# Kernel optimization log

Hardware: AMD Instinct MI355X
Metric: run time of the kernel (lower is better)

Reference implementation:

```python
import jax, jax.numpy as jnp
import numpy as np

EPSILON = 0.1
MAX_ITERATIONS = 100


def setup_inputs() -> dict:
    key = jax.random.key(0)
    k1, k2 = jax.random.split(key)
    x = jax.random.normal(k1, (16, 3, 2048), dtype=jnp.float32)
    y = jax.random.normal(k2, (16, 3, 2048), dtype=jnp.float32)
    return {"x": x, "y": y}


def reference(x, y):
    # x, y: (B, D, N) channels-first point clouds -> (B, N, D)
    xt = jnp.swapaxes(x, 1, 2)
    yt = jnp.swapaxes(y, 1, 2)
    B, N, _ = xt.shape
    # squared euclidean cost: (B, N, N)
    x2 = jnp.sum(xt * xt, axis=-1)  # (B, N)
    y2 = jnp.sum(yt * yt, axis=-1)  # (B, N)
    C = x2[:, :, None] + y2[:, None, :] - 2.0 * jnp.einsum('bnd,bmd->bnm', xt, yt)
    C = jnp.maximum(C, 0.0)  # cdist clamps negatives from cancellation
    K = jnp.exp(-C / EPSILON)

    inv_n = 1.0 / N
    u0 = jnp.full((B, N), inv_n, dtype=x.dtype)
    v0 = jnp.full((B, N), inv_n, dtype=x.dtype)

    def step(carry, _):
        u, _v = carry
        v = inv_n / (jnp.einsum('bnm,bn->bm', K, u) + 1e-8)  # K^T u
        u = inv_n / (jnp.einsum('bnm,bm->bn', K, v) + 1e-8)  # K v
        return (u, v), None

    (u, v), _ = jax.lax.scan(step, (u0, v0), None, length=MAX_ITERATIONS)
    # sum(plan * C) / B where plan = u[:,:,None] * K * v[:,None,:]
    return jnp.einsum('bn,bnm,bm->', u, K * C, v) / B
```

## Files before the change

kernel.cpp:

```cpp
#include <hip/hip_runtime.h>

#define NB 16
#define NN 2048
#define G  64
#define ITERS 100

typedef float v2f __attribute__((ext_vector_type(2)));

static constexpr float INV_N = 1.0f / (float)NN;
static constexpr float NEG_INV_EPS = -10.0f;

__device__ __forceinline__ float fastrcp(float x) { return __builtin_amdgcn_rcpf(x); }

__device__ __forceinline__ void dec4(unsigned int u, float& f0, float& f1, float& f2, float& f3) {
    v2f lo = __builtin_amdgcn_cvt_pk_f32_fp8((int)u, false);
    v2f hi = __builtin_amdgcn_cvt_pk_f32_fp8((int)u, true);
    f0 = lo[0]; f1 = lo[1]; f2 = hi[0]; f3 = hi[1];
}

__global__ __launch_bounds__(256) void build_K(const float* __restrict__ x,
                                               const float* __restrict__ y,
                                               unsigned char* __restrict__ K8,
                                               float* __restrict__ INVS) {
    const int n = blockIdx.x, b = blockIdx.y, tid = threadIdx.x;
    const int w = tid >> 6, l = tid & 63;
    const float* xb = x + (size_t)b * 3 * NN;
    const float* yb = y + (size_t)b * 3 * NN;
    const float x0 = xb[n], x1 = xb[NN + n], x2 = xb[2 * NN + n];
    const float xs = x0 * x0 + x1 * x1 + x2 * x2;
    const int m0 = tid * 8;

    const float4 a0 = *(const float4*)(yb + m0);
    const float4 a1 = *(const float4*)(yb + m0 + 4);
    const float4 b0 = *(const float4*)(yb + NN + m0);
    const float4 b1 = *(const float4*)(yb + NN + m0 + 4);
    const float4 c0 = *(const float4*)(yb + 2 * NN + m0);
    const float4 c1 = *(const float4*)(yb + 2 * NN + m0 + 4);
    const float yy0[8] = {a0.x, a0.y, a0.z, a0.w, a1.x, a1.y, a1.z, a1.w};
    const float yy1[8] = {b0.x, b0.y, b0.z, b0.w, b1.x, b1.y, b1.z, b1.w};
    const float yy2[8] = {c0.x, c0.y, c0.z, c0.w, c1.x, c1.y, c1.z, c1.w};

    float k[8];
#pragma unroll
    for (int j = 0; j < 8; ++j) {
        const float ys  = yy0[j] * yy0[j] + yy1[j] * yy1[j] + yy2[j] * yy2[j];
        const float dot = x0 * yy0[j] + x1 * yy1[j] + x2 * yy2[j];
        const float C   = fmaxf(xs + ys - 2.0f * dot, 0.0f);
        k[j] = __expf(NEG_INV_EPS * C);
    }

    float mx = fmaxf(fmaxf(fmaxf(k[0], k[1]), fmaxf(k[2], k[3])),
                     fmaxf(fmaxf(k[4], k[5]), fmaxf(k[6], k[7])));
#pragma unroll
    for (int off = 32; off > 0; off >>= 1) mx = fmaxf(mx, __shfl_xor(mx, off, 64));
    __shared__ float red[4];
    if (l == 0) red[w] = mx;
    __syncthreads();
    mx = fmaxf(fmaxf(red[0], red[1]), fmaxf(red[2], red[3]));
    mx = fmaxf(mx, 1e-30f);
    const int e = (int)((__float_as_uint(mx) >> 23) & 0xffu) - 127;
    const float sc = __uint_as_float((unsigned)(127 - e) << 23);
    if (tid == 0) INVS[b * NN + n] = __uint_as_float((unsigned)(127 + e) << 23);

    int p0 = __builtin_amdgcn_cvt_pk_fp8_f32(k[0] * sc, k[1] * sc, 0, false);
    p0     = __builtin_amdgcn_cvt_pk_fp8_f32(k[2] * sc, k[3] * sc, p0, true);
    int p1 = __builtin_amdgcn_cvt_pk_fp8_f32(k[4] * sc, k[5] * sc, 0, false);
    p1     = __builtin_amdgcn_cvt_pk_fp8_f32(k[6] * sc, k[7] * sc, p1, true);
    uint2 pk; pk.x = (unsigned)p0; pk.y = (unsigned)p1;
    *(uint2*)(K8 + ((size_t)(b * NN + n)) * NN + m0) = pk;
}

__global__ __launch_bounds__(256) void reduce_v(const float* __restrict__ PART,
                                                float* __restrict__ VV) {
    const int t = blockIdx.x * 256 + threadIdx.x;
    const int b = t >> 9;
    const int m4 = (t & 511) << 2;
    const float* p = PART + (size_t)(b * G) * NN + m4;
    float s0 = 0, s1 = 0, s2 = 0, s3 = 0;
#pragma unroll 8
    for (int g = 0; g < G; ++g) {
        const float4 q = *(const float4*)(p + (size_t)g * NN);
        s0 += q.x; s1 += q.y; s2 += q.z; s3 += q.w;
    }
    float4 o;
    o.x = INV_N * fastrcp(s0 + 1e-8f);
    o.y = INV_N * fastrcp(s1 + 1e-8f);
    o.z = INV_N * fastrcp(s2 + 1e-8f);
    o.w = INV_N * fastrcp(s3 + 1e-8f);
    *(float4*)(VV + (size_t)b * NN + m4) = o;
}

#define DOT16(kk, vv) {                                                        \
    float f0_, f1_, f2_, f3_;                                                  \
    dec4(kk.x, f0_, f1_, f2_, f3_);                                            \
    d0 = fmaf(f0_, vv[0], d0);  d1 = fmaf(f1_, vv[1], d1);                     \
    d2 = fmaf(f2_, vv[2], d2);  d3 = fmaf(f3_, vv[3], d3);                     \
    dec4(kk.y, f0_, f1_, f2_, f3_);                                            \
    d0 = fmaf(f0_, vv[4], d0);  d1 = fmaf(f1_, vv[5], d1);                     \
    d2 = fmaf(f2_, vv[6], d2);  d3 = fmaf(f3_, vv[7], d3);                     \
    dec4(kk.z, f0_, f1_, f2_, f3_);                                            \
    d0 = fmaf(f0_, vv[8], d0);  d1 = fmaf(f1_, vv[9], d1);                     \
    d2 = fmaf(f2_, vv[10], d2); d3 = fmaf(f3_, vv[11], d3);                    \
    dec4(kk.w, f0_, f1_, f2_, f3_);                                            \
    d0 = fmaf(f0_, vv[12], d0); d1 = fmaf(f1_, vv[13], d1);                    \
    d2 = fmaf(f2_, vv[14], d2); d3 = fmaf(f3_, vv[15], d3); }

#define ACC16(kk, aa, uu) {                                                    \
    float f0_, f1_, f2_, f3_;                                                  \
    dec4(kk.x, f0_, f1_, f2_, f3_);                                            \
    aa[0] = fmaf(f0_, uu, aa[0]);   aa[1] = fmaf(f1_, uu, aa[1]);              \
    aa[2] = fmaf(f2_, uu, aa[2]);   aa[3] = fmaf(f3_, uu, aa[3]);              \
    dec4(kk.y, f0_, f1_, f2_, f3_);                                            \
    aa[4] = fmaf(f0_, uu, aa[4]);   aa[5] = fmaf(f1_, uu, aa[5]);              \
    aa[6] = fmaf(f2_, uu, aa[6]);   aa[7] = fmaf(f3_, uu, aa[7]);              \
    dec4(kk.z, f0_, f1_, f2_, f3_);                                            \
    aa[8] = fmaf(f0_, uu, aa[8]);   aa[9] = fmaf(f1_, uu, aa[9]);              \
    aa[10] = fmaf(f2_, uu, aa[10]); aa[11] = fmaf(f3_, uu, aa[11]);            \
    dec4(kk.w, f0_, f1_, f2_, f3_);                                            \
    aa[12] = fmaf(f0_, uu, aa[12]); aa[13] = fmaf(f1_, uu, aa[13]);            \
    aa[14] = fmaf(f2_, uu, aa[14]); aa[15] = fmaf(f3_, uu, aa[15]); }

__global__ __launch_bounds__(256) void fused_pass(const unsigned char* __restrict__ K8,
                                                  const float* __restrict__ VV,
                                                  const float* __restrict__ INVS,
                                                  float* __restrict__ u_out,
                                                  float* __restrict__ PART,
                                                  int first) {
    const int g = blockIdx.x, b = blockIdx.y, tid = threadIdx.x;
    const int w = tid >> 6, l = tid & 63;

    float v[2][16];
    if (!first) {
        const float* vb = VV + b * NN + l * 16;
#pragma unroll
        for (int h = 0; h < 2; ++h) {
            const float4 q0 = *(const float4*)(vb + h * 1024);
            const float4 q1 = *(const float4*)(vb + h * 1024 + 4);
            const float4 q2 = *(const float4*)(vb + h * 1024 + 8);
            const float4 q3 = *(const float4*)(vb + h * 1024 + 12);
            v[h][0]  = q0.x; v[h][1]  = q0.y; v[h][2]  = q0.z; v[h][3]  = q0.w;
            v[h][4]  = q1.x; v[h][5]  = q1.y; v[h][6]  = q1.z; v[h][7]  = q1.w;
            v[h][8]  = q2.x; v[h][9]  = q2.y; v[h][10] = q2.z; v[h][11] = q2.w;
            v[h][12] = q3.x; v[h][13] = q3.y; v[h][14] = q3.z; v[h][15] = q3.w;
        }
    }

    float acc0[16], acc1[16];
#pragma unroll
    for (int j = 0; j < 16; ++j) { acc0[j] = 0.0f; acc1[j] = 0.0f; }

    const int row0 = g * 32 + w * 8;
    const unsigned char* Kb = K8 + ((size_t)(b * NN + row0)) * NN + l * 16;
    const float* invp = INVS + b * NN + row0;

#pragma unroll
    for (int rp = 0; rp < 4; ++rp) {
        const unsigned char* pA = Kb + (size_t)(2 * rp) * NN;
        const unsigned char* pB = pA + NN;
        const uint4 kA0 = *(const uint4*)(pA);
        const uint4 kA1 = *(const uint4*)(pA + 1024);
        const uint4 kB0 = *(const uint4*)(pB);
        const uint4 kB1 = *(const uint4*)(pB + 1024);
        const float invsA = invp[2 * rp];
        const float invsB = invp[2 * rp + 1];

        float uwA, uwB;
        if (first) {
            uwA = INV_N * invsA;
            uwB = INV_N * invsB;
        } else {
            float d0 = 0, d1 = 0, d2 = 0, d3 = 0;
            DOT16(kA0, v[0]); DOT16(kA1, v[1]);
            float dA = (d0 + d1) + (d2 + d3);
            d0 = 0; d1 = 0; d2 = 0; d3 = 0;
            DOT16(kB0, v[0]); DOT16(kB1, v[1]);
            float dB = (d0 + d1) + (d2 + d3);
#pragma unroll
            for (int off = 32; off > 0; off >>= 1) {
                dA += __shfl_xor(dA, off, 64);
                dB += __shfl_xor(dB, off, 64);
            }
            uwA = INV_N * fastrcp(dA * invsA + 1e-8f) * invsA;
            uwB = INV_N * fastrcp(dB * invsB + 1e-8f) * invsB;
        }
        if (l == 0) {
            u_out[b * NN + row0 + 2 * rp]     = uwA;
            u_out[b * NN + row0 + 2 * rp + 1] = uwB;
        }
        ACC16(kA0, acc0, uwA); ACC16(kA1, acc1, uwA);
        ACC16(kB0, acc0, uwB); ACC16(kB1, acc1, uwB);
    }

    __shared__ float lds[4][NN];
    {
        float* dst = &lds[w][l * 16];
        *(float4*)(dst)          = make_float4(acc0[0],  acc0[1],  acc0[2],  acc0[3]);
        *(float4*)(dst + 4)      = make_float4(acc0[4],  acc0[5],  acc0[6],  acc0[7]);
        *(float4*)(dst + 8)      = make_float4(acc0[8],  acc0[9],  acc0[10], acc0[11]);
        *(float4*)(dst + 12)     = make_float4(acc0[12], acc0[13], acc0[14], acc0[15]);
        *(float4*)(dst + 1024)      = make_float4(acc1[0],  acc1[1],  acc1[2],  acc1[3]);
        *(float4*)(dst + 1024 + 4)  = make_float4(acc1[4],  acc1[5],  acc1[6],  acc1[7]);
        *(float4*)(dst + 1024 + 8)  = make_float4(acc1[8],  acc1[9],  acc1[10], acc1[11]);
        *(float4*)(dst + 1024 + 12) = make_float4(acc1[12], acc1[13], acc1[14], acc1[15]);
    }
    __syncthreads();
    float o[8];
#pragma unroll
    for (int j = 0; j < 8; ++j)
        o[j] = (lds[0][tid * 8 + j] + lds[1][tid * 8 + j]) +
               (lds[2][tid * 8 + j] + lds[3][tid * 8 + j]);
    float* p = PART + ((size_t)(b * G + g)) * NN + tid * 8;
    *(float4*)(p)     = make_float4(o[0], o[1], o[2], o[3]);
    *(float4*)(p + 4) = make_float4(o[4], o[5], o[6], o[7]);
}

__global__ __launch_bounds__(256) void final_sum(const unsigned char* __restrict__ K8,
                                                 const float* __restrict__ x,
                                                 const float* __restrict__ y,
                                                 const float* __restrict__ VV,
                                                 const float* __restrict__ u_in,
                                                 float* __restrict__ out) {
    const int g = blockIdx.x, b = blockIdx.y, tid = threadIdx.x;
    const int w = tid >> 6, l = tid & 63;
    const float* vb = VV + b * NN;

    float v[4][8];
#pragma unroll
    for (int s = 0; s < 4; ++s) {
        const float4 p0 = *(const float4*)(vb + s * 512 + l * 8);
        const float4 p1 = *(const float4*)(vb + s * 512 + l * 8 + 4);
        v[s][0] = p0.x; v[s][1] = p0.y; v[s][2] = p0.z; v[s][3] = p0.w;
        v[s][4] = p1.x; v[s][5] = p1.y; v[s][6] = p1.z; v[s][7] = p1.w;
    }

    const float* xb = x + (size_t)b * 3 * NN;
    const float* yb = y + (size_t)b * 3 * NN;
    float lacc = 0.0f;

    for (int r = 0; r < 8; ++r) {
        const int n = g * 32 + w * 8 + r;
        const float x0 = xb[n], x1 = xb[NN + n], x2 = xb[2 * NN + n];
        const float xs = x0 * x0 + x1 * x1 + x2 * x2;
        const float uwn = u_in[b * NN + n];
        const unsigned char* Kp = K8 + ((size_t)(b * NN + n)) * NN + l * 8;
        float racc = 0.0f;
#pragma unroll
        for (int s = 0; s < 4; ++s) {
            const int m0 = s * 512 + l * 8;
            const uint2 kv = *(const uint2*)(Kp + s * 512);
            float ky[8];
            dec4(kv.x, ky[0], ky[1], ky[2], ky[3]);
            dec4(kv.y, ky[4], ky[5], ky[6], ky[7]);
            const float4 a0 = *(const float4*)(yb + m0);
            const float4 a1 = *(const float4*)(yb + m0 + 4);
            const float4 b0 = *(const float4*)(yb + NN + m0);
            const float4 b1 = *(const float4*)(yb + NN + m0 + 4);
            const float4 c0 = *(const float4*)(yb + 2 * NN + m0);
            const float4 c1 = *(const float4*)(yb + 2 * NN + m0 + 4);
            const float yy0[8] = {a0.x, a0.y, a0.z, a0.w, a1.x, a1.y, a1.z, a1.w};
            const float yy1[8] = {b0.x, b0.y, b0.z, b0.w, b1.x, b1.y, b1.z, b1.w};
            const float yy2[8] = {c0.x, c0.y, c0.z, c0.w, c1.x, c1.y, c1.z, c1.w};
#pragma unroll
            for (int j = 0; j < 8; ++j) {
                const float ys  = yy0[j] * yy0[j] + yy1[j] * yy1[j] + yy2[j] * yy2[j];
                const float dot = x0 * yy0[j] + x1 * yy1[j] + x2 * yy2[j];
                const float C   = fmaxf(xs + ys - 2.0f * dot, 0.0f);
                racc = fmaf(ky[j] * C, v[s][j], racc);
            }
        }
        lacc = fmaf(uwn, racc, lacc);
    }
#pragma unroll
    for (int off = 32; off > 0; off >>= 1) lacc += __shfl_xor(lacc, off, 64);
    __shared__ float red[4];
    if (l == 0) red[w] = lacc;
    __syncthreads();
    if (tid == 0) atomicAdd(out, (red[0] + red[1] + red[2] + red[3]) * (1.0f / (float)NB));
}

extern "C" void kernel_launch(void* const* d_in, const int* in_sizes, int n_in,
                              void* d_out, int out_size, void* d_ws, size_t ws_size,
                              hipStream_t stream) {
    const float* x = (const float*)d_in[0];
    const float* y = (const float*)d_in[1];
    float* out = (float*)d_out;
    char* ws = (char*)d_ws;

    unsigned char* K8 = (unsigned char*)ws;
    const size_t KBYTES = (size_t)NB * NN * NN;
    float* PART = (float*)(ws + KBYTES);
    const size_t PARTN = (size_t)NB * G * NN;
    float* VV   = PART + PARTN;
    float* ub   = VV + (size_t)NB * NN;
    float* INVS = ub + (size_t)NB * NN;

    hipMemsetAsync(out, 0, sizeof(float), stream);

    build_K<<<dim3(NN, NB), 256, 0, stream>>>(x, y, K8, INVS);

    fused_pass<<<dim3(G, NB), 256, 0, stream>>>(K8, VV, INVS, ub, PART, 1);
    for (int i = 0; i < ITERS; ++i) {
        reduce_v<<<dim3(NB * NN / 4 / 256), 256, 0, stream>>>(PART, VV);
        fused_pass<<<dim3(G, NB), 256, 0, stream>>>(K8, VV, INVS, ub, PART, 0);
    }
    final_sum<<<dim3(G, NB), 256, 0, stream>>>(K8, x, y, VV, ub, out);
}
```

Baseline: 3.022 ms.

## Stream K rows through an LDS ring with async global-to-LDS loads

Rewrites the fused_pass row loop so each wave stages its eight fp8 K rows through a four-slot LDS ring filled by global_load_lds, waiting on vmcnt per row so loads overlap the dot-product and accumulate math. The same LDS is reused for the cross-wave fold, and the u values are written by lanes 0-7 in one store instead of per-row writes from lane 0. reduce_v is also changed to one scalar column per thread with four times as many blocks, which raises parallelism but drops vectorized loads. The manual waitcnt and sched_barrier placement adds fragility and extra LDS traffic in exchange for latency hiding.

```diff
diff --git a/kernel.cpp b/kernel.cpp
--- a/kernel.cpp
+++ b/kernel.cpp
@@ -73,21 +73,12 @@
 __global__ __launch_bounds__(256) void reduce_v(const float* __restrict__ PART,
                                                 float* __restrict__ VV) {
     const int t = blockIdx.x * 256 + threadIdx.x;
-    const int b = t >> 9;
-    const int m4 = (t & 511) << 2;
-    const float* p = PART + (size_t)(b * G) * NN + m4;
-    float s0 = 0, s1 = 0, s2 = 0, s3 = 0;
+    const int b = t >> 11, m = t & (NN - 1);
+    const float* p = PART + (size_t)(b * G) * NN + m;
+    float s = 0.0f;
 #pragma unroll 8
-    for (int g = 0; g < G; ++g) {
-        const float4 q = *(const float4*)(p + (size_t)g * NN);
-        s0 += q.x; s1 += q.y; s2 += q.z; s3 += q.w;
-    }
-    float4 o;
-    o.x = INV_N * fastrcp(s0 + 1e-8f);
-    o.y = INV_N * fastrcp(s1 + 1e-8f);
-    o.z = INV_N * fastrcp(s2 + 1e-8f);
-    o.w = INV_N * fastrcp(s3 + 1e-8f);
-    *(float4*)(VV + (size_t)b * NN + m4) = o;
+    for (int g = 0; g < G; ++g) s += p[(size_t)g * NN];
+    VV[t] = INV_N * fastrcp(s + 1e-8f);
 }
 
 #define DOT16(kk, vv) {                                                        \
@@ -120,6 +111,39 @@
     aa[12] = fmaf(f0_, uu, aa[12]); aa[13] = fmaf(f1_, uu, aa[13]);            \
     aa[14] = fmaf(f2_, uu, aa[14]); aa[15] = fmaf(f3_, uu, aa[15]); }
 
+#define ROWSTEP(R, WN, INVSR) {                                                           \
+    asm volatile("s_waitcnt vmcnt(" #WN ")" ::: "memory");                                \
+    __builtin_amdgcn_sched_barrier(0);                                                    \
+    const uint4 k0 = *(const uint4*)(ring + ((R) & 3) * 2048 + l * 16);                   \
+    const uint4 k1 = *(const uint4*)(ring + ((R) & 3) * 2048 + 1024 + l * 16);            \
+    float d = 0.0f;                                                                       \
+    if (!first) {                                                                         \
+        float d0 = 0, d1 = 0, d2 = 0, d3 = 0;                                             \
+        DOT16(k0, v[0]); DOT16(k1, v[1]);                                                 \
+        d = (d0 + d1) + (d2 + d3);                                                        \
+    }                                                                                     \
+    asm volatile("s_waitcnt lgkmcnt(0)" ::: "memory");                                    \
+    __builtin_amdgcn_sched_barrier(0);                                                    \
+    if ((R) < 4) {                                                                        \
+        __builtin_amdgcn_global_load_lds(                                                 \
+            (const __attribute__((address_space(1))) void*)(rowg + (size_t)((R) + 4) * NN + l * 16),        \
+            (__attribute__((address_space(3))) void*)(ring + ((R) & 3) * 2048), 16, 0, 0);                  \
+        __builtin_amdgcn_global_load_lds(                                                 \
+            (const __attribute__((address_space(1))) void*)(rowg + (size_t)((R) + 4) * NN + 1024 + l * 16), \
+            (__attribute__((address_space(3))) void*)(ring + ((R) & 3) * 2048 + 1024), 16, 0, 0);           \
+    }                                                                                     \
+    const float invs = (INVSR);                                                           \
+    float uw;                                                                             \
+    if (first) {                                                                          \
+        uw = INV_N * invs;                                                                \
+    } else {                                                                              \
+        for (int off = 32; off > 0; off >>= 1) d += __shfl_xor(d, off, 64);               \
+        uw = INV_N * fastrcp(d * invs + 1e-8f) * invs;                                    \
+    }                                                                                     \
+    uwsel = (l == (R)) ? uw : uwsel;                                                      \
+    ACC16(k0, acc0, uw); ACC16(k1, acc1, uw);                                             \
+}
+
 __global__ __launch_bounds__(256) void fused_pass(const unsigned char* __restrict__ K8,
                                                   const float* __restrict__ VV,
                                                   const float* __restrict__ INVS,
@@ -128,6 +152,9 @@
                                                   int first) {
     const int g = blockIdx.x, b = blockIdx.y, tid = threadIdx.x;
     const int w = tid >> 6, l = tid & 63;
+
+    __shared__ __align__(16) unsigned char smem[32768];
+    unsigned char* ring = smem + w * 8192;
 
     float v[2][16];
     if (!first) {
@@ -150,65 +177,53 @@
     for (int j = 0; j < 16; ++j) { acc0[j] = 0.0f; acc1[j] = 0.0f; }
 
     const int row0 = g * 32 + w * 8;
-    const unsigned char* Kb = K8 + ((size_t)(b * NN + row0)) * NN + l * 16;
-    const float* invp = INVS + b * NN + row0;
-
-#pragma unroll
-    for (int rp = 0; rp < 4; ++rp) {
-        const unsigned char* pA = Kb + (size_t)(2 * rp) * NN;
-        const unsigned char* pB = pA + NN;
-        const uint4 kA0 = *(const uint4*)(pA);
-        const uint4 kA1 = *(const uint4*)(pA + 1024);
-        const uint4 kB0 = *(const uint4*)(pB);
-        const uint4 kB1 = *(const uint4*)(pB + 1024);
-        const float invsA = invp[2 * rp];
-        const float invsB = invp[2 * rp + 1];
-
-        float uwA, uwB;
-        if (first) {
-            uwA = INV_N * invsA;
-            uwB = INV_N * invsB;
-        } else {
-            float d0 = 0, d1 = 0, d2 = 0, d3 = 0;
-            DOT16(kA0, v[0]); DOT16(kA1, v[1]);
-            float dA = (d0 + d1) + (d2 + d3);
-            d0 = 0; d1 = 0; d2 = 0; d3 = 0;
-            DOT16(kB0, v[0]); DOT16(kB1, v[1]);
-            float dB = (d0 + d1) + (d2 + d3);
-#pragma unroll
-            for (int off = 32; off > 0; off >>= 1) {
-                dA += __shfl_xor(dA, off, 64);
-                dB += __shfl_xor(dB, off, 64);
-            }
-            uwA = INV_N * fastrcp(dA * invsA + 1e-8f) * invsA;
-            uwB = INV_N * fastrcp(dB * invsB + 1e-8f) * invsB;
-        }
-        if (l == 0) {
-            u_out[b * NN + row0 + 2 * rp]     = uwA;
-            u_out[b * NN + row0 + 2 * rp + 1] = uwB;
-        }
-        ACC16(kA0, acc0, uwA); ACC16(kA1, acc1, uwA);
-        ACC16(kB0, acc0, uwB); ACC16(kB1, acc1, uwB);
-    }
-
-    __shared__ float lds[4][NN];
-    {
-        float* dst = &lds[w][l * 16];
-        *(float4*)(dst)          = make_float4(acc0[0],  acc0[1],  acc0[2],  acc0[3]);
-        *(float4*)(dst + 4)      = make_float4(acc0[4],  acc0[5],  acc0[6],  acc0[7]);
-        *(float4*)(dst + 8)      = make_float4(acc0[8],  acc0[9],  acc0[10], acc0[11]);
-        *(float4*)(dst + 12)     = make_float4(acc0[12], acc0[13], acc0[14], acc0[15]);
-        *(float4*)(dst + 1024)      = make_float4(acc1[0],  acc1[1],  acc1[2],  acc1[3]);
-        *(float4*)(dst + 1024 + 4)  = make_float4(acc1[4],  acc1[5],  acc1[6],  acc1[7]);
-        *(float4*)(dst + 1024 + 8)  = make_float4(acc1[8],  acc1[9],  acc1[10], acc1[11]);
-        *(float4*)(dst + 1024 + 12) = make_float4(acc1[12], acc1[13], acc1[14], acc1[15]);
+    const unsigned char* rowg = K8 + ((size_t)(b * NN + row0)) * NN;
+    const float4 iv0 = *(const float4*)(INVS + b * NN + row0);
+    const float4 iv1 = *(const float4*)(INVS + b * NN + row0 + 4);
+
+    asm volatile("s_waitcnt vmcnt(0)" ::: "memory");
+    __builtin_amdgcn_sched_barrier(0);
+
+#pragma unroll
+    for (int rr = 0; rr < 4; ++rr) {
+#pragma unroll
+        for (int h = 0; h < 2; ++h)
+            __builtin_amdgcn_global_load_lds(
+                (const __attribute__((address_space(1))) void*)(rowg + (size_t)rr * NN + h * 1024 + l * 16),
+                (__attribute__((address_space(3))) void*)(ring + rr * 2048 + h * 1024), 16, 0, 0);
+    }
+
+    float uwsel = 0.0f;
+    ROWSTEP(0, 6, iv0.x)
+    ROWSTEP(1, 6, iv0.y)
+    ROWSTEP(2, 6, iv0.z)
+    ROWSTEP(3, 6, iv0.w)
+    ROWSTEP(4, 6, iv1.x)
+    ROWSTEP(5, 4, iv1.y)
+    ROWSTEP(6, 2, iv1.z)
+    ROWSTEP(7, 0, iv1.w)
+
+    if (l < 8) u_out[b * NN + row0 + l] = uwsel;
+
+    float* fold = (float*)(smem + w * 8192);
+#pragma unroll
+    for (int h = 0; h < 2; ++h) {
+        float* dst = fold + h * 1024 + l * 16;
+        const float* a = h ? acc1 : acc0;
+        *(float4*)(dst)      = make_float4(a[0],  a[1],  a[2],  a[3]);
+        *(float4*)(dst + 4)  = make_float4(a[4],  a[5],  a[6],  a[7]);
+        *(float4*)(dst + 8)  = make_float4(a[8],  a[9],  a[10], a[11]);
+        *(float4*)(dst + 12) = make_float4(a[12], a[13], a[14], a[15]);
     }
     __syncthreads();
+    const float* f0 = (const float*)(smem);
+    const float* f1 = (const float*)(smem + 8192);
+    const float* f2 = (const float*)(smem + 16384);
+    const float* f3 = (const float*)(smem + 24576);
     float o[8];
 #pragma unroll
     for (int j = 0; j < 8; ++j)
-        o[j] = (lds[0][tid * 8 + j] + lds[1][tid * 8 + j]) +
-               (lds[2][tid * 8 + j] + lds[3][tid * 8 + j]);
+        o[j] = (f0[tid * 8 + j] + f1[tid * 8 + j]) + (f2[tid * 8 + j] + f3[tid * 8 + j]);
     float* p = PART + ((size_t)(b * G + g)) * NN + tid * 8;
     *(float4*)(p)     = make_float4(o[0], o[1], o[2], o[3]);
     *(float4*)(p + 4) = make_float4(o[4], o[5], o[6], o[7]);
@@ -300,7 +315,7 @@
 
     fused_pass<<<dim3(G, NB), 256, 0, stream>>>(K8, VV, INVS, ub, PART, 1);
     for (int i = 0; i < ITERS; ++i) {
-        reduce_v<<<dim3(NB * NN / 4 / 256), 256, 0, stream>>>(PART, VV);
+        reduce_v<<<dim3(NB * NN / 256), 256, 0, stream>>>(PART, VV);
         fused_pass<<<dim3(G, NB), 256, 0, stream>>>(K8, VV, INVS, ub, PART, 0);
     }
     final_sum<<<dim3(G, NB), 256, 0, stream>>>(K8, x, y, VV, ub, out);
```

Measured after the change: 3.671 ms. +21.5%, slower.
